# Kernel optimization log

Measured on AMD Instinct MI355X. Metric: run time of the kernel, lower is better.

Reference implementation:

```python
import jax, jax.numpy as jnp
import numpy as np
from jax import lax

WS = 8       # RSA window size
HEADS = 8    # GSA heads
EPS_LN = 1e-5

def conv1x1(x, w):  # x:(b,c,h,w), w:(o,c)
    return jnp.einsum('bchw,oc->bohw', x, w)

def dwconv3x3(x, w):  # w:(c,1,3,3) depthwise
    return lax.conv_general_dilated(x, w, (1, 1), ((1, 1), (1, 1)),
                                    dimension_numbers=('NCHW', 'OIHW', 'NCHW'),
                                    feature_group_count=x.shape[1])

def layernorm(x, w, b):  # WithBias LayerNorm over channel dim
    mu = x.mean(axis=1, keepdims=True)
    var = ((x - mu) ** 2).mean(axis=1, keepdims=True)
    return (x - mu) / jnp.sqrt(var + EPS_LN) * w[None, :, None, None] + b[None, :, None, None]

def l2norm(x):  # F.normalize(dim=-1)
    n = jnp.sqrt(jnp.sum(x * x, axis=-1, keepdims=True))
    return x / jnp.maximum(n, 1e-12)

def window_part(x, ws):  # (b,c,H,W) -> (b,nwin,ws*ws,c)
    b, c, H, W = x.shape
    x = x.reshape(b, c, H // ws, ws, W // ws, ws)
    x = x.transpose(0, 2, 4, 3, 5, 1)
    return x.reshape(b, (H // ws) * (W // ws), ws * ws, c)

def window_merge(x, ws, H, W):  # inverse of window_part
    b, nwin, _, c = x.shape
    x = x.reshape(b, H // ws, W // ws, ws, ws, c)
    x = x.transpose(0, 5, 1, 3, 2, 4)
    return x.reshape(b, c, H, W)

def rsa(x, qkv_w, dw_w, proj_w, temp):
    b, c, H, W = x.shape
    sh = WS // 2  # torch: roll by -wsize//2 = -4
    x_ = jnp.roll(x, (-sh, -sh), axis=(2, 3))
    qkv = dwconv3x3(conv1x1(x_, qkv_w), dw_w)
    q, k, v = jnp.split(qkv, 3, axis=1)
    q = l2norm(window_part(q, WS))
    k = l2norm(window_part(k, WS))
    v = window_part(v, WS)
    # attn[c,d] = sum_p q[p,c] k[p,d]; relu instead of softmax
    attn = jax.nn.relu(jnp.einsum('bnpc,bnpd->bncd', q, k) * temp[0, 0, 0])
    out = jnp.einsum('bnpc,bncd->bnpd', v, attn)
    out = window_merge(out, WS, H, W)
    out = jnp.roll(out, (sh, sh), axis=(2, 3))
    return conv1x1(out, proj_w), attn

def gsa(x, qkv_w, dw_w, proj_w, temp):
    b, c, H, W = x.shape
    cp = c // HEADS
    qkv = dwconv3x3(conv1x1(x, qkv_w), dw_w)
    q, k, v = jnp.split(qkv, 3, axis=1)
    heads = lambda t: t.reshape(b, HEADS, cp, H * W)
    q = l2norm(heads(q)); k = l2norm(heads(k)); v = heads(v)
    attn = jax.nn.relu(jnp.einsum('bhcn,bhdn->bhcd', q, k) * temp[0, 0, 0])
    out = jnp.einsum('bhcd,bhdn->bhcn', attn, v)  # (b,head,cp,HW)
    # rearrange 'b head c hw -> b (head c) h w' then 'b (head c) h w -> b (c head) h w'
    y = out.reshape(b, HEADS, cp, H, W).transpose(0, 2, 1, 3, 4).reshape(b, c, H, W)
    return conv1x1(y, proj_w), attn

def ffn(x, in_w, dw_w, out_w):  # Restormer gated-dconv FFN, bias=False
    h2 = dwconv3x3(conv1x1(x, in_w), dw_w)
    x1, x2 = jnp.split(h2, 2, axis=1)
    return conv1x1(jax.nn.gelu(x1, approximate=False) * x2, out_w)


def setup_inputs() -> dict:
    key = jax.random.key(0)
    B, C, H, W = 8, 64, 128, 128
    HID = int(C * 2.66)  # 170
    ks = jax.random.split(key, 20)
    g = lambda k, shp, s: (jax.random.normal(k, shp, dtype=jnp.float32) * s)
    d = {
        'x': g(ks[0], (B, C, H, W), 1.0),
        'ln_s0_w': jnp.ones((C,), jnp.float32), 'ln_s0_b': jnp.zeros((C,), jnp.float32),
        'ln_s2_w': jnp.ones((C,), jnp.float32), 'ln_s2_b': jnp.zeros((C,), jnp.float32),
        'rsa_qkv_w': g(ks[1], (3 * C, C), 0.05), 'rsa_dw_w': g(ks[2], (3 * C, 1, 3, 3), 0.1),
        'rsa_proj_w': g(ks[3], (C, C), 0.05), 'rsa_temp': jnp.ones((1, 1, 1), jnp.float32),
        'ffd_s_in_w': g(ks[4], (2 * HID, C), 0.05), 'ffd_s_dw_w': g(ks[5], (2 * HID, 1, 3, 3), 0.1),
        'ffd_s_out_w': g(ks[6], (C, HID), 0.05),
        'ln_c0_w': jnp.ones((C,), jnp.float32), 'ln_c0_b': jnp.zeros((C,), jnp.float32),
        'ln_c2_w': jnp.ones((C,), jnp.float32), 'ln_c2_b': jnp.zeros((C,), jnp.float32),
        'gsa_qkv_w': g(ks[7], (3 * C, C), 0.05), 'gsa_dw_w': g(ks[8], (3 * C, 1, 3, 3), 0.1),
        'gsa_proj_w': g(ks[9], (C, C), 0.05), 'gsa_temp': jnp.ones((1, 1, 1), jnp.float32),
        'ffd_c_in_w': g(ks[10], (2 * HID, C), 0.05), 'ffd_c_dw_w': g(ks[11], (2 * HID, 1, 3, 3), 0.1),
        'ffd_c_out_w': g(ks[12], (C, HID), 0.05),
    }
    return d


def reference(x, ln_s0_w, ln_s0_b, ln_s2_w, ln_s2_b,
              rsa_qkv_w, rsa_dw_w, rsa_proj_w, rsa_temp,
              ffd_s_in_w, ffd_s_dw_w, ffd_s_out_w,
              ln_c0_w, ln_c0_b, ln_c2_w, ln_c2_b,
              gsa_qkv_w, gsa_dw_w, gsa_proj_w, gsa_temp,
              ffd_c_in_w, ffd_c_dw_w, ffd_c_out_w):
    # FDT block, shared_depth=1 (i==0 branches only)
    x_, _ = rsa(layernorm(x, ln_s0_w, ln_s0_b), rsa_qkv_w, rsa_dw_w, rsa_proj_w, rsa_temp)
    x = ffn(layernorm(x_ + x, ln_s2_w, ln_s2_b), ffd_s_in_w, ffd_s_dw_w, ffd_s_out_w) + x_
    x_, _ = gsa(layernorm(x, ln_c0_w, ln_c0_b), gsa_qkv_w, gsa_dw_w, gsa_proj_w, gsa_temp)
    x = ffn(layernorm(x_ + x, ln_c2_w, ln_c2_b), ffd_c_in_w, ffd_c_dw_w, ffd_c_out_w) + x_
    return x
```

## Files before the change

kernel.cpp:

```cpp
#include <hip/hip_runtime.h>
#include <hip/hip_bf16.h>
#include <math.h>

#define DI __device__ __forceinline__

constexpr int B = 8, C = 64, H = 128, W = 128, N = H * W;
constexpr int HID = 170;
constexpr int QKVC = 3 * C;

typedef _Float16 half8 __attribute__((ext_vector_type(8)));
typedef _Float16 half4v __attribute__((ext_vector_type(4)));
typedef float f32x4 __attribute__((ext_vector_type(4)));

DI float gelu_fast(float v) {
    return v / (1.0f + __expf(-1.5957691216057308f * (v + 0.044715f * v * v * v)));
}

__global__ __launch_bounds__(64) void wpack_kernel(
    const float* __restrict__ Wm, const float* __restrict__ lnsc,
    int OREAL, int KREAL, int KT, _Float16* __restrict__ out)
{
    int f = blockIdx.x, l = threadIdx.x;
    int mt = f / KT, kt = f % KT;
    int row = mt * 16 + (l & 15);
    int col0 = kt * 32 + (l >> 4) * 8;
    half8 v;
#pragma unroll
    for (int i = 0; i < 8; ++i) {
        int col = col0 + i;
        float w = (row < OREAL && col < KREAL) ? Wm[row * KREAL + col] : 0.f;
        if (lnsc && col < KREAL) w *= lnsc[col];
        v[i] = (_Float16)w;
    }
    *(half8*)(out + (size_t)f * 512 + l * 8) = v;
}

__global__ __launch_bounds__(64) void wbias_kernel(
    const float* __restrict__ Wm, const float* __restrict__ lnb,
    int OREAL, int OPAD, float* __restrict__ biasv)
{
    int o = blockIdx.x * 64 + threadIdx.x;
    if (o >= OPAD) return;
    float s = 0.f;
    if (o < OREAL) {
#pragma unroll
        for (int c = 0; c < 64; ++c) s += Wm[o * 64 + c] * lnb[c];
    }
    biasv[o] = s;
}

__global__ __launch_bounds__(512) void weffpack_kernel(
    const float* __restrict__ weff, _Float16* __restrict__ out)
{
    int b = blockIdx.x;
    int f = threadIdx.x >> 6, l = threadIdx.x & 63;
    int mt = f >> 1, kt = f & 1;
    int row = mt * 16 + (l & 15);
    int col0 = kt * 32 + (l >> 4) * 8;
    const float* wb = weff + (size_t)b * 4096;
    half8 v;
#pragma unroll
    for (int i = 0; i < 8; ++i) v[i] = (_Float16)wb[row * 64 + col0 + i];
    *(half8*)(out + ((size_t)b * 8 + f) * 512 + l * 8) = v;
}

template<int MT, int OREAL, bool PRIM16, bool ADDIN>
__global__ __launch_bounds__(256, 1) void lngemm_kernel(
    const void* __restrict__ Xv, const float* __restrict__ Xadd,
    const float* __restrict__ biasv,
    const _Float16* __restrict__ Wp, _Float16* __restrict__ outp)
{
    __shared__ _Float16 stash[4][MT][16][66];
    int t = threadIdx.x, lane = t & 63, mg = t >> 6;
    int pbase = blockIdx.x * 64;
    int b = pbase >> 14, nb = pbase & (N - 1);
    int g = lane >> 4, lm = lane & 15;
    int krow0 = g * 8;

    half8 a[MT][2];
    const _Float16* wb = Wp + (size_t)(mg * MT * 2) * 512 + lane * 8;
#pragma unroll
    for (int mt = 0; mt < MT; ++mt)
#pragma unroll
        for (int kt = 0; kt < 2; ++kt)
            a[mt][kt] = *(const half8*)(wb + (mt * 2 + kt) * 512);

    int rowbase = mg * (MT * 16);
    const float* bp = biasv + rowbase + g * 4;

    const float*    xb32 = PRIM16 ? nullptr : ((const float*)Xv) + (size_t)b * 64 * N;
    const _Float16* xb16 = PRIM16 ? ((const _Float16*)Xv) + (size_t)b * 64 * N : nullptr;
    const float* ab = ADDIN ? (Xadd + (size_t)b * 64 * N) : nullptr;

#pragma unroll
    for (int cg = 0; cg < 4; ++cg) {
        int col = nb + cg * 16 + lm;
        float vv[2][8];
        float sm = 0.f, ss = 0.f;
#pragma unroll
        for (int kt = 0; kt < 2; ++kt)
#pragma unroll
            for (int i = 0; i < 8; ++i) {
                int c = kt * 32 + krow0 + i;
                float v = PRIM16 ? (float)xb16[(size_t)c * N + col] : xb32[(size_t)c * N + col];
                if (ADDIN) v += ab[(size_t)c * N + col];
                vv[kt][i] = v; sm += v; ss += v * v;
            }
        sm += __shfl_xor(sm, 16); ss += __shfl_xor(ss, 16);
        sm += __shfl_xor(sm, 32); ss += __shfl_xor(ss, 32);
        float mu = sm * (1.0f / 64.0f);
        float var = ss * (1.0f / 64.0f) - mu * mu;
        float rstd = rsqrtf(var + 1e-5f);
        half8 bf[2];
#pragma unroll
        for (int kt = 0; kt < 2; ++kt)
#pragma unroll
            for (int i = 0; i < 8; ++i)
                bf[kt][i] = (_Float16)((vv[kt][i] - mu) * rstd);

        f32x4 acc[MT];
#pragma unroll
        for (int mt = 0; mt < MT; ++mt) acc[mt] = *(const f32x4*)(bp + mt * 16);
#pragma unroll
        for (int kt = 0; kt < 2; ++kt)
#pragma unroll
            for (int mt = 0; mt < MT; ++mt)
                acc[mt] = __builtin_amdgcn_mfma_f32_16x16x32_f16(a[mt][kt], bf[kt], acc[mt], 0, 0, 0);

#pragma unroll
        for (int mt = 0; mt < MT; ++mt)
#pragma unroll
            for (int r = 0; r < 4; ++r)
                stash[mg][mt][g * 4 + r][cg * 16 + lm] = (_Float16)acc[mt][r];
    }
    __syncthreads();

    int row = lane >> 2, chunk = lane & 3;
#pragma unroll
    for (int mt = 0; mt < MT; ++mt) {
        int orow = rowbase + mt * 16 + row;
        if ((4 * MT * 16 == OREAL) || orow < OREAL) {
            half8 v0 = *(const half8*)&stash[mg][mt][row][chunk * 16];
            half8 v1 = *(const half8*)&stash[mg][mt][row][chunk * 16 + 8];
            _Float16* op = outp + ((size_t)b * OREAL + orow) * N + nb + chunk * 16;
            *(half8*)op = v0;
            *(half8*)(op + 8) = v1;
        }
    }
}

template<int MT, int KT, int MG, int NSTRIP, int CIN, int OREAL, int XROWS,
         bool PBW, bool OUT32, bool RESID>
__global__ __launch_bounds__(256, 1) void gemm_kernel(
    const _Float16* __restrict__ X, const _Float16* __restrict__ Wp,
    const _Float16* __restrict__ resid, void* __restrict__ outv)
{
    constexpr int PG = 4 / MG;
    constexpr int PPB = PG * 16 * NSTRIP;
    int t = threadIdx.x;
    int lane = t & 63, wv = t >> 6;
    int mg = wv % MG, pg = wv / MG;
    int pbase = blockIdx.x * PPB;
    int b = pbase >> 14, nb = pbase & (N - 1);

    half8 a[MT][KT];
    const _Float16* wb = Wp + ((size_t)(PBW ? b * (MG * MT * KT) : 0) + mg * MT * KT) * 512 + lane * 8;
#pragma unroll
    for (int mt = 0; mt < MT; ++mt)
#pragma unroll
        for (int kt = 0; kt < KT; ++kt)
            a[mt][kt] = *(const half8*)(wb + (mt * KT + kt) * 512);

    const _Float16* xb = X + (size_t)b * XROWS * N;
    int krow0 = (lane >> 4) * 8;

    for (int s = 0; s < NSTRIP; ++s) {
        int col = nb + (s * PG + pg) * 16 + (lane & 15);
        const _Float16* xp = xb + col;
        half8 bf[KT];
#pragma unroll
        for (int kt = 0; kt < KT; ++kt)
#pragma unroll
            for (int i = 0; i < 8; ++i) {
                int c = kt * 32 + krow0 + i;
                if (KT * 32 <= CIN || c < CIN) bf[kt][i] = xp[(size_t)c * N];
                else bf[kt][i] = (_Float16)0.f;
            }
        f32x4 acc[MT];
#pragma unroll
        for (int mt = 0; mt < MT; ++mt) acc[mt] = (f32x4){0.f, 0.f, 0.f, 0.f};
#pragma unroll
        for (int kt = 0; kt < KT; ++kt)
#pragma unroll
            for (int mt = 0; mt < MT; ++mt)
                acc[mt] = __builtin_amdgcn_mfma_f32_16x16x32_f16(a[mt][kt], bf[kt], acc[mt], 0, 0, 0);

        int orow0 = mg * (MT * 16) + (lane >> 4) * 4;
#pragma unroll
        for (int mt = 0; mt < MT; ++mt)
#pragma unroll
            for (int r = 0; r < 4; ++r) {
                int orow = orow0 + mt * 16 + r;
                bool ok = (MG * MT * 16 == OREAL) || (orow < OREAL);
                if (ok) {
                    size_t oidx = ((size_t)b * OREAL + orow) * N + col;
                    if constexpr (OUT32) {
                        float vv = acc[mt][r];
                        if constexpr (RESID) vv += (float)resid[((size_t)b * 64 + orow) * N + col];
                        ((float*)outv)[oidx] = vv;
                    } else {
                        ((_Float16*)outv)[oidx] = (_Float16)acc[mt][r];
                    }
                }
            }
    }
}

template<bool ROLLWM>
__global__ __launch_bounds__(256, 1) void dw16_kernel(
    const _Float16* __restrict__ in, const float* __restrict__ w,
    _Float16* __restrict__ out)
{
    int bc = blockIdx.y;
    int c = bc % 192;
    int n0 = (blockIdx.x * 256 + threadIdx.x) * 8;
    int y = n0 >> 7, x0 = n0 & 127;
    const _Float16* ib = in + (size_t)bc * N;
    const float* wr = w + c * 9;
    _Float16 wh[9];
#pragma unroll
    for (int i = 0; i < 9; ++i) wh[i] = (_Float16)wr[i];

    half8 acc = {0, 0, 0, 0, 0, 0, 0, 0};
#pragma unroll
    for (int r = 0; r < 3; ++r) {
        int yy = y - 1 + r;
        if (yy < 0 || yy > 127) continue;
        half8 sL, m, sR;
        if (!ROLLWM) {
            const _Float16* rp = ib + yy * W + x0;
            m = *(const half8*)rp;
            half8 pv = {0, 0, 0, 0, 0, 0, 0, 0};
            half8 nv = {0, 0, 0, 0, 0, 0, 0, 0};
            pv[7] = (x0 > 0) ? rp[-1] : (_Float16)0.f;
            nv[0] = (x0 < 120) ? rp[8] : (_Float16)0.f;
            sL = __builtin_shufflevector(pv, m, 7, 8, 9, 10, 11, 12, 13, 14);
            sR = __builtin_shufflevector(m, nv, 1, 2, 3, 4, 5, 6, 7, 8);
        } else {
            int sy = (yy + 4) & 127;
            const _Float16* rp = ib + sy * W;
            if (x0 <= 112) {
                half8 b0 = *(const half8*)(rp + x0);
                half8 b1 = *(const half8*)(rp + x0 + 8);
                sL = __builtin_shufflevector(b0, b1, 3, 4, 5, 6, 7, 8, 9, 10);
                m  = __builtin_shufflevector(b0, b1, 4, 5, 6, 7, 8, 9, 10, 11);
                sR = __builtin_shufflevector(b0, b1, 5, 6, 7, 8, 9, 10, 11, 12);
                if (x0 == 0) sL[0] = (_Float16)0.f;
            } else {
                _Float16 tmp[10];
#pragma unroll
                for (int j = 0; j < 10; ++j) {
                    int xx = 119 + j;
                    tmp[j] = (xx <= 127) ? rp[(xx + 4) & 127] : (_Float16)0.f;
                }
#pragma unroll
                for (int j = 0; j < 8; ++j) { sL[j] = tmp[j]; m[j] = tmp[j + 1]; sR[j] = tmp[j + 2]; }
            }
        }
        acc += sL * wh[r * 3 + 0] + m * wh[r * 3 + 1] + sR * wh[r * 3 + 2];
    }
    if (ROLLWM) {
        int win = ((y >> 3) << 4) | (x0 >> 3);
        int p = (y & 7) << 3;
        *(half8*)(out + (size_t)bc * N + win * 64 + p) = acc;
    } else {
        *(half8*)(out + (size_t)bc * N + n0) = acc;
    }
}

__global__ __launch_bounds__(256, 3) void rsa_win_kernel(
    const _Float16* __restrict__ qkv, const float* __restrict__ temp_p,
    const _Float16* __restrict__ pwp, _Float16* __restrict__ out)
{
    __shared__ _Float16 qT[64][72];
    __shared__ _Float16 kT[64][72];
    __shared__ _Float16 vP[64][76];
    __shared__ _Float16 aT[64][76];
    __shared__ _Float16 oP[64][76];
    __shared__ float tnorm[128];
    __shared__ _Float16 wsc[64];
    int blk = blockIdx.x, b = blk >> 8, win = blk & 255;
    int t = threadIdx.x, lane = t & 63, wv = t >> 6;
    int g = lane >> 4, lm = lane & 15;

    half8 pa0 = *(const half8*)(pwp + (size_t)(wv * 2 + 0) * 512 + lane * 8);
    half8 pa1 = *(const half8*)(pwp + (size_t)(wv * 2 + 1) * 512 + lane * 8);

    const _Float16* base = qkv + (size_t)b * QKVC * N + win * 64;
    {
        int c = t >> 2, q0 = (t & 3) * 16;
        const _Float16* pq = base + (size_t)c * N + q0;
        half8 a0 = *(const half8*)(pq);
        half8 a1 = *(const half8*)(pq + 8);
        *(half8*)&qT[c][q0] = a0;
        *(half8*)&qT[c][q0 + 8] = a1;
        const _Float16* pk = base + (size_t)(64 + c) * N + q0;
        half8 b0 = *(const half8*)(pk);
        half8 b1 = *(const half8*)(pk + 8);
        *(half8*)&kT[c][q0] = b0;
        *(half8*)&kT[c][q0 + 8] = b1;
        const _Float16* pv = base + (size_t)(128 + c) * N + q0;
        half8 v0 = *(const half8*)(pv);
        half8 v1 = *(const half8*)(pv + 8);
#pragma unroll
        for (int j = 0; j < 8; ++j) vP[q0 + j][c] = v0[j];
#pragma unroll
        for (int j = 0; j < 8; ++j) vP[q0 + 8 + j][c] = v1[j];
    }
    __syncthreads();
    if (t < 128) {
        int p = t & 63;
        float s = 0.f;
        if (t < 64) {
#pragma unroll
            for (int c = 0; c < 64; ++c) { float a = (float)qT[c][p]; s += a * a; }
        } else {
#pragma unroll
            for (int c = 0; c < 64; ++c) { float a = (float)kT[c][p]; s += a * a; }
        }
        tnorm[t] = s;
    }
    __syncthreads();
    if (t < 64) {
        float r = temp_p[0] / (fmaxf(sqrtf(tnorm[t]), 1e-12f) * fmaxf(sqrtf(tnorm[64 + t]), 1e-12f));
        wsc[t] = (_Float16)r;
    }
    __syncthreads();

    {
        half8 aq0 = *(const half8*)&qT[wv * 16 + lm][g * 8];
        half8 aq1 = *(const half8*)&qT[wv * 16 + lm][32 + g * 8];
        half8 ws0 = *(const half8*)&wsc[g * 8];
        half8 ws1 = *(const half8*)&wsc[32 + g * 8];
#pragma unroll
        for (int nt = 0; nt < 4; ++nt) {
            int d = nt * 16 + lm;
            half8 bk0 = *(const half8*)&kT[d][g * 8] * ws0;
            half8 bk1 = *(const half8*)&kT[d][32 + g * 8] * ws1;
            f32x4 acc = {0.f, 0.f, 0.f, 0.f};
            acc = __builtin_amdgcn_mfma_f32_16x16x32_f16(aq0, bk0, acc, 0, 0, 0);
            acc = __builtin_amdgcn_mfma_f32_16x16x32_f16(aq1, bk1, acc, 0, 0, 0);
#pragma unroll
            for (int r = 0; r < 4; ++r)
                aT[wv * 16 + g * 4 + r][d] = (_Float16)fmaxf(acc[r], 0.f);
        }
    }
    __syncthreads();

    {
        half8 a20, a21;
#pragma unroll
        for (int i = 0; i < 8; ++i) {
            a20[i] = aT[g * 8 + i][wv * 16 + lm];
            a21[i] = aT[32 + g * 8 + i][wv * 16 + lm];
        }
#pragma unroll
        for (int nt = 0; nt < 4; ++nt) {
            int p = nt * 16 + lm;
            half4v x0 = *(const half4v*)&vP[p][g * 8];
            half4v x1 = *(const half4v*)&vP[p][g * 8 + 4];
            half4v x2 = *(const half4v*)&vP[p][32 + g * 8];
            half4v x3 = *(const half4v*)&vP[p][32 + g * 8 + 4];
            half8 b20, b21;
#pragma unroll
            for (int j = 0; j < 4; ++j) { b20[j] = x0[j]; b20[4 + j] = x1[j]; b21[j] = x2[j]; b21[4 + j] = x3[j]; }
            f32x4 acc = {0.f, 0.f, 0.f, 0.f};
            acc = __builtin_amdgcn_mfma_f32_16x16x32_f16(a20, b20, acc, 0, 0, 0);
            acc = __builtin_amdgcn_mfma_f32_16x16x32_f16(a21, b21, acc, 0, 0, 0);
#pragma unroll
            for (int r = 0; r < 4; ++r)
                oP[p][wv * 16 + g * 4 + r] = (_Float16)acc[r];
        }
    }
    __syncthreads();

    {
        int y0 = (win >> 4) * 8, x0w = (win & 15) * 8;
        _Float16* ob = out + (size_t)b * C * N;
#pragma unroll
        for (int nt = 0; nt < 4; ++nt) {
            int p = nt * 16 + lm;
            half4v x0 = *(const half4v*)&oP[p][g * 8];
            half4v x1 = *(const half4v*)&oP[p][g * 8 + 4];
            half4v x2 = *(const half4v*)&oP[p][32 + g * 8];
            half4v x3 = *(const half4v*)&oP[p][32 + g * 8 + 4];
            half8 b30, b31;
#pragma unroll
            for (int j = 0; j < 4; ++j) { b30[j] = x0[j]; b30[4 + j] = x1[j]; b31[j] = x2[j]; b31[4 + j] = x3[j]; }
            f32x4 acc = {0.f, 0.f, 0.f, 0.f};
            acc = __builtin_amdgcn_mfma_f32_16x16x32_f16(pa0, b30, acc, 0, 0, 0);
            acc = __builtin_amdgcn_mfma_f32_16x16x32_f16(pa1, b31, acc, 0, 0, 0);
            int gy = (y0 + (p >> 3) + 4) & 127;
            int gx = (x0w + (p & 7) + 4) & 127;
#pragma unroll
            for (int r = 0; r < 4; ++r)
                ob[(size_t)(wv * 16 + g * 4 + r) * N + gy * W + gx] = (_Float16)acc[r];
        }
    }
}

__global__ __launch_bounds__(256, 1) void ffn_b_kernel(
    const _Float16* __restrict__ hid,
    const float* __restrict__ dww,
    _Float16* __restrict__ gated)
{
    int bc = blockIdx.y;
    int b = bc / 170, c = bc % 170;
    int n0 = (blockIdx.x * 256 + threadIdx.x) * 8;
    int y = n0 >> 7, x0 = n0 & 127;
    const _Float16* pa = hid + ((size_t)b * 340 + c) * N;
    const _Float16* pb = pa + (size_t)170 * N;
    const float* wa = dww + c * 9;
    const float* wbp = wa + 170 * 9;
    _Float16 wha[9], whb[9];
#pragma unroll
    for (int i = 0; i < 9; ++i) { wha[i] = (_Float16)wa[i]; whb[i] = (_Float16)wbp[i]; }

    half8 accA = {0, 0, 0, 0, 0, 0, 0, 0};
    half8 accB = {0, 0, 0, 0, 0, 0, 0, 0};
#pragma unroll
    for (int r = 0; r < 3; ++r) {
        int yy = y - 1 + r;
        if (yy < 0 || yy > 127) continue;
        {
            const _Float16* ra = pa + yy * W + x0;
            half8 m = *(const half8*)ra;
            half8 pv = {0, 0, 0, 0, 0, 0, 0, 0};
            half8 nv = {0, 0, 0, 0, 0, 0, 0, 0};
            pv[7] = (x0 > 0) ? ra[-1] : (_Float16)0.f;
            nv[0] = (x0 < 120) ? ra[8] : (_Float16)0.f;
            half8 sL = __builtin_shufflevector(pv, m, 7, 8, 9, 10, 11, 12, 13, 14);
            half8 sR = __builtin_shufflevector(m, nv, 1, 2, 3, 4, 5, 6, 7, 8);
            accA += sL * wha[r * 3 + 0] + m * wha[r * 3 + 1] + sR * wha[r * 3 + 2];
        }
        {
            const _Float16* rb = pb + yy * W + x0;
            half8 m = *(const half8*)rb;
            half8 pv = {0, 0, 0, 0, 0, 0, 0, 0};
            half8 nv = {0, 0, 0, 0, 0, 0, 0, 0};
            pv[7] = (x0 > 0) ? rb[-1] : (_Float16)0.f;
            nv[0] = (x0 < 120) ? rb[8] : (_Float16)0.f;
            half8 sL = __builtin_shufflevector(pv, m, 7, 8, 9, 10, 11, 12, 13, 14);
            half8 sR = __builtin_shufflevector(m, nv, 1, 2, 3, 4, 5, 6, 7, 8);
            accB += sL * whb[r * 3 + 0] + m * whb[r * 3 + 1] + sR * whb[r * 3 + 2];
        }
    }
    half8 o;
#pragma unroll
    for (int i = 0; i < 8; ++i) {
        float a = (float)accA[i];
        float g2 = (float)accB[i];
        o[i] = (_Float16)(gelu_fast(a) * g2);
    }
    *(half8*)(gated + ((size_t)b * 170 + c) * N + n0) = o;
}

__global__ __launch_bounds__(256, 1) void gsa_part_kernel(
    const _Float16* __restrict__ qkv, float* __restrict__ part)
{
    int bh = blockIdx.y, chunk = blockIdx.x;
    int b = bh >> 3, h = bh & 7;
    int t = threadIdx.x;
    const _Float16* qb = qkv + ((size_t)b * QKVC + h * 8) * N;
    const _Float16* kb = qb + (size_t)64 * N;
    float acc[80];
#pragma unroll
    for (int j = 0; j < 80; ++j) acc[j] = 0.f;
    for (int i = 0; i < 8; ++i) {
        int n = chunk * 2048 + i * 256 + t;
        float qv[8], kv[8];
#pragma unroll
        for (int c = 0; c < 8; ++c) { qv[c] = (float)qb[(size_t)c * N + n]; kv[c] = (float)kb[(size_t)c * N + n]; }
#pragma unroll
        for (int c = 0; c < 8; ++c) {
            acc[64 + c] += qv[c] * qv[c];
            acc[72 + c] += kv[c] * kv[c];
#pragma unroll
            for (int d = 0; d < 8; ++d) acc[c * 8 + d] += qv[c] * kv[d];
        }
    }
#pragma unroll
    for (int j = 0; j < 80; ++j) {
        float v = acc[j];
#pragma unroll
        for (int m = 1; m < 64; m <<= 1) v += __shfl_xor(v, m, 64);
        acc[j] = v;
    }
    __shared__ float red[4 * 80];
    if ((t & 63) == 0) {
#pragma unroll
        for (int j = 0; j < 80; ++j) red[(t >> 6) * 80 + j] = acc[j];
    }
    __syncthreads();
    if (t < 80) {
        float s = red[t] + red[80 + t] + red[160 + t] + red[240 + t];
        part[((size_t)bh * 8 + chunk) * 80 + t] = s;
    }
}

__global__ __launch_bounds__(128) void gsa_fin_kernel(
    const float* __restrict__ part, const float* __restrict__ temp_p,
    float* __restrict__ attn)
{
    int bh = blockIdx.x;
    int t = threadIdx.x;
    __shared__ float red[80];
    if (t < 80) {
        float s = 0.f;
        for (int ch = 0; ch < 8; ++ch) s += part[((size_t)bh * 8 + ch) * 80 + t];
        red[t] = s;
    }
    __syncthreads();
    if (t < 64) {
        int c = t >> 3, d = t & 7;
        float S  = red[c * 8 + d];
        float qn = fmaxf(sqrtf(red[64 + c]), 1e-12f);
        float kn = fmaxf(sqrtf(red[72 + d]), 1e-12f);
        attn[(size_t)bh * 64 + t] = fmaxf(temp_p[0] * S / (qn * kn), 0.f);
    }
}

__global__ __launch_bounds__(64) void weff_kernel(
    const float* __restrict__ attn, const float* __restrict__ pw,
    float* __restrict__ weff)
{
    int b = blockIdx.x;
    int o = threadIdx.x;
    __shared__ float al[512];
    for (int idx = o; idx < 512; idx += 64) al[idx] = attn[(size_t)b * 512 + idx];
    __syncthreads();
    for (int hd = 0; hd < 64; ++hd) {
        int h = hd >> 3, d = hd & 7;
        float acc = 0.f;
#pragma unroll
        for (int c = 0; c < 8; ++c)
            acc += pw[o * 64 + c * 8 + h] * al[h * 64 + c * 8 + d];
        weff[((size_t)b * 64 + o) * 64 + hd] = acc;
    }
}

__global__ void sentinel_kernel(float* out, int n) {
    int i = blockIdx.x * 256 + threadIdx.x;
    if (i < n) out[i] = 12345.0f;
}

extern "C" void kernel_launch(void* const* d_in, const int* in_sizes, int n_in,
                              void* d_out, int out_size, void* d_ws, size_t ws_size,
                              hipStream_t stream)
{
    const float* x         = (const float*)d_in[0];
    const float* ln_s0_w   = (const float*)d_in[1];
    const float* ln_s0_b   = (const float*)d_in[2];
    const float* ln_s2_w   = (const float*)d_in[3];
    const float* ln_s2_b   = (const float*)d_in[4];
    const float* rsa_qkv_w = (const float*)d_in[5];
    const float* rsa_dw_w  = (const float*)d_in[6];
    const float* rsa_proj_w= (const float*)d_in[7];
    const float* rsa_temp  = (const float*)d_in[8];
    const float* ffs_in_w  = (const float*)d_in[9];
    const float* ffs_dw_w  = (const float*)d_in[10];
    const float* ffs_out_w = (const float*)d_in[11];
    const float* ln_c0_w   = (const float*)d_in[12];
    const float* ln_c0_b   = (const float*)d_in[13];
    const float* ln_c2_w   = (const float*)d_in[14];
    const float* ln_c2_b   = (const float*)d_in[15];
    const float* gsa_qkv_w = (const float*)d_in[16];
    const float* gsa_dw_w  = (const float*)d_in[17];
    const float* gsa_proj_w= (const float*)d_in[18];
    const float* gsa_temp  = (const float*)d_in[19];
    const float* ffc_in_w  = (const float*)d_in[20];
    const float* ffc_dw_w  = (const float*)d_in[21];
    const float* ffc_out_w = (const float*)d_in[22];
    float* outp = (float*)d_out;

    char* ws = (char*)d_ws;
    _Float16* tmp192 = (_Float16*)(ws + 0);
    _Float16* Qbuf16 = (_Float16*)(ws + 50331648ull);
    _Float16* hidA   = (_Float16*)(ws + 0);
    _Float16* gated  = (_Float16*)(ws + 89128960ull);
    _Float16* wp_rsap= (_Float16*)(ws + 133693440ull);
    _Float16* S2h    = (_Float16*)(ws + 134217728ull);
    float*    part   = (float*)(ws + 167772160ull);
    float*    attn_s = (float*)(ws + 168427520ull);
    float*    weffb  = (float*)(ws + 168443904ull);
    _Float16* wp_rsa = (_Float16*)(ws + 168574976ull);
    _Float16* wp_gsa = (_Float16*)(ws + 168599552ull);
    _Float16* wp_fsi = (_Float16*)(ws + 168624128ull);
    _Float16* wp_fci = (_Float16*)(ws + 168673280ull);
    _Float16* wp_fso = (_Float16*)(ws + 168722432ull);
    _Float16* wp_fco = (_Float16*)(ws + 168747008ull);
    _Float16* wp_pbw = (_Float16*)(ws + 168771584ull);
    float*    wb_rsa = (float*)(ws + 168837120ull);
    float*    wb_gsa = (float*)(ws + 168838144ull);
    float*    wb_fsi = (float*)(ws + 168839168ull);
    float*    wb_fci = (float*)(ws + 168841216ull);
    if (ws_size < 168843264ull) {
        int n = out_size < 4096 ? out_size : 4096;
        sentinel_kernel<<<16, 256, 0, stream>>>(outp, n);
        return;
    }

    dim3 blk256(256);

    wpack_kernel<<<24, 64, 0, stream>>>(rsa_qkv_w, ln_s0_w, 192, 64, 2, wp_rsa);
    wpack_kernel<<<24, 64, 0, stream>>>(gsa_qkv_w, ln_c0_w, 192, 64, 2, wp_gsa);
    wpack_kernel<<<48, 64, 0, stream>>>(ffs_in_w, ln_s2_w, 340, 64, 2, wp_fsi);
    wpack_kernel<<<48, 64, 0, stream>>>(ffc_in_w, ln_c2_w, 340, 64, 2, wp_fci);
    wpack_kernel<<<24, 64, 0, stream>>>(ffs_out_w, nullptr, 64, 170, 6, wp_fso);
    wpack_kernel<<<24, 64, 0, stream>>>(ffc_out_w, nullptr, 64, 170, 6, wp_fco);
    wpack_kernel<<<8, 64, 0, stream>>>(rsa_proj_w, nullptr, 64, 64, 2, wp_rsap);
    wbias_kernel<<<3, 64, 0, stream>>>(rsa_qkv_w, ln_s0_b, 192, 192, wb_rsa);
    wbias_kernel<<<3, 64, 0, stream>>>(gsa_qkv_w, ln_c0_b, 192, 192, wb_gsa);
    wbias_kernel<<<6, 64, 0, stream>>>(ffs_in_w, ln_s2_b, 340, 384, wb_fsi);
    wbias_kernel<<<6, 64, 0, stream>>>(ffc_in_w, ln_c2_b, 340, 384, wb_fci);

    lngemm_kernel<3, 192, false, false><<<2048, blk256, 0, stream>>>(x, nullptr, wb_rsa, wp_rsa, tmp192);
    dw16_kernel<true><<<dim3(8, B * 192), blk256, 0, stream>>>(tmp192, rsa_dw_w, Qbuf16);
    rsa_win_kernel<<<2048, blk256, 0, stream>>>(Qbuf16, rsa_temp, wp_rsap, S2h);
    lngemm_kernel<6, 340, true, true><<<2048, blk256, 0, stream>>>(S2h, x, wb_fsi, wp_fsi, hidA);
    ffn_b_kernel<<<dim3(8, B * 170), blk256, 0, stream>>>(hidA, ffs_dw_w, gated);
    gemm_kernel<2, 6, 2, 2, 170, 64, 170, false, true, true>
        <<<2048, blk256, 0, stream>>>(gated, wp_fso, S2h, outp);

    lngemm_kernel<3, 192, false, false><<<2048, blk256, 0, stream>>>(outp, nullptr, wb_gsa, wp_gsa, tmp192);
    dw16_kernel<false><<<dim3(8, B * 192), blk256, 0, stream>>>(tmp192, gsa_dw_w, Qbuf16);
    gsa_part_kernel<<<dim3(8, 64), blk256, 0, stream>>>(Qbuf16, part);
    gsa_fin_kernel<<<64, dim3(128), 0, stream>>>(part, gsa_temp, attn_s);
    weff_kernel<<<8, dim3(64), 0, stream>>>(attn_s, gsa_proj_w, weffb);
    weffpack_kernel<<<8, dim3(512), 0, stream>>>(weffb, wp_pbw);
    gemm_kernel<4, 2, 1, 1, 64, 64, 192, true, false, false>
        <<<2048, blk256, 0, stream>>>(Qbuf16 + (size_t)128 * N, wp_pbw, nullptr, S2h);
    lngemm_kernel<6, 340, true, true><<<2048, blk256, 0, stream>>>(S2h, outp, wb_fci, wp_fci, hidA);
    ffn_b_kernel<<<dim3(8, B * 170), blk256, 0, stream>>>(hidA, ffc_dw_w, gated);
    gemm_kernel<2, 6, 2, 2, 170, 64, 170, false, true, true>
        <<<2048, blk256, 0, stream>>>(gated, wp_fco, S2h, outp);
}
```

Before: 393.4 us.

## Store intermediate block output in fp16 and widen FFN depthwise per-thread work

The first FFN output GEMM now writes the intermediate activation as fp16 (X2h) instead of fp32 into the output buffer. The following GSA layernorm-GEMM and the second FFN layernorm-GEMM read it as fp16, which halves traffic for that tensor. The FFN depthwise+gate kernel now processes 16 pixels per thread on a 3D grid, reusing halo loads and halving the block count. The fp16 intermediate adds rounding error to the residual path.

```diff
diff --git a/kernel.cpp b/kernel.cpp
--- a/kernel.cpp
+++ b/kernel.cpp
@@ -64,9 +64,9 @@
     *(half8*)(out + ((size_t)b * 8 + f) * 512 + l * 8) = v;
 }
 
-template<int MT, int OREAL, bool PRIM16, bool ADDIN>
+template<int MT, int OREAL, bool PRIM16, bool RES16, bool ADDIN>
 __global__ __launch_bounds__(256, 1) void lngemm_kernel(
-    const void* __restrict__ Xv, const float* __restrict__ Xadd,
+    const void* __restrict__ Xv, const void* __restrict__ Xaddv,
     const float* __restrict__ biasv,
     const _Float16* __restrict__ Wp, _Float16* __restrict__ outp)
 {
@@ -90,7 +90,8 @@
 
     const float*    xb32 = PRIM16 ? nullptr : ((const float*)Xv) + (size_t)b * 64 * N;
     const _Float16* xb16 = PRIM16 ? ((const _Float16*)Xv) + (size_t)b * 64 * N : nullptr;
-    const float* ab = ADDIN ? (Xadd + (size_t)b * 64 * N) : nullptr;
+    const float*    ab32 = (ADDIN && !RES16) ? ((const float*)Xaddv) + (size_t)b * 64 * N : nullptr;
+    const _Float16* ab16 = (ADDIN && RES16) ? ((const _Float16*)Xaddv) + (size_t)b * 64 * N : nullptr;
 
 #pragma unroll
     for (int cg = 0; cg < 4; ++cg) {
@@ -103,7 +104,7 @@
             for (int i = 0; i < 8; ++i) {
                 int c = kt * 32 + krow0 + i;
                 float v = PRIM16 ? (float)xb16[(size_t)c * N + col] : xb32[(size_t)c * N + col];
-                if (ADDIN) v += ab[(size_t)c * N + col];
+                if (ADDIN) v += RES16 ? (float)ab16[(size_t)c * N + col] : ab32[(size_t)c * N + col];
                 vv[kt][i] = v; sm += v; ss += v * v;
             }
         sm += __shfl_xor(sm, 16); ss += __shfl_xor(ss, 16);
@@ -204,13 +205,10 @@
                 bool ok = (MG * MT * 16 == OREAL) || (orow < OREAL);
                 if (ok) {
                     size_t oidx = ((size_t)b * OREAL + orow) * N + col;
-                    if constexpr (OUT32) {
-                        float vv = acc[mt][r];
-                        if constexpr (RESID) vv += (float)resid[((size_t)b * 64 + orow) * N + col];
-                        ((float*)outv)[oidx] = vv;
-                    } else {
-                        ((_Float16*)outv)[oidx] = (_Float16)acc[mt][r];
-                    }
+                    float vv = acc[mt][r];
+                    if constexpr (RESID) vv += (float)resid[((size_t)b * 64 + orow) * N + col];
+                    if constexpr (OUT32) ((float*)outv)[oidx] = vv;
+                    else                 ((_Float16*)outv)[oidx] = (_Float16)vv;
                 }
             }
     }
@@ -414,9 +412,8 @@
     const float* __restrict__ dww,
     _Float16* __restrict__ gated)
 {
-    int bc = blockIdx.y;
-    int b = bc / 170, c = bc % 170;
-    int n0 = (blockIdx.x * 256 + threadIdx.x) * 8;
+    int c = blockIdx.y, b = blockIdx.z;
+    int n0 = (blockIdx.x * 256 + threadIdx.x) * 16;
     int y = n0 >> 7, x0 = n0 & 127;
     const _Float16* pa = hid + ((size_t)b * 340 + c) * N;
     const _Float16* pb = pa + (size_t)170 * N;
@@ -426,43 +423,52 @@
 #pragma unroll
     for (int i = 0; i < 9; ++i) { wha[i] = (_Float16)wa[i]; whb[i] = (_Float16)wbp[i]; }
 
-    half8 accA = {0, 0, 0, 0, 0, 0, 0, 0};
-    half8 accB = {0, 0, 0, 0, 0, 0, 0, 0};
+    half8 aA0 = {0,0,0,0,0,0,0,0}, aA1 = {0,0,0,0,0,0,0,0};
+    half8 aB0 = {0,0,0,0,0,0,0,0}, aB1 = {0,0,0,0,0,0,0,0};
 #pragma unroll
     for (int r = 0; r < 3; ++r) {
         int yy = y - 1 + r;
         if (yy < 0 || yy > 127) continue;
         {
             const _Float16* ra = pa + yy * W + x0;
-            half8 m = *(const half8*)ra;
-            half8 pv = {0, 0, 0, 0, 0, 0, 0, 0};
-            half8 nv = {0, 0, 0, 0, 0, 0, 0, 0};
-            pv[7] = (x0 > 0) ? ra[-1] : (_Float16)0.f;
-            nv[0] = (x0 < 120) ? ra[8] : (_Float16)0.f;
-            half8 sL = __builtin_shufflevector(pv, m, 7, 8, 9, 10, 11, 12, 13, 14);
-            half8 sR = __builtin_shufflevector(m, nv, 1, 2, 3, 4, 5, 6, 7, 8);
-            accA += sL * wha[r * 3 + 0] + m * wha[r * 3 + 1] + sR * wha[r * 3 + 2];
+            half8 m0 = *(const half8*)ra;
+            half8 m1 = *(const half8*)(ra + 8);
+            half8 pv = {0,0,0,0,0,0,0,0};
+            half8 nv = {0,0,0,0,0,0,0,0};
+            pv[7] = (x0 > 0)   ? ra[-1] : (_Float16)0.f;
+            nv[0] = (x0 < 112) ? ra[16] : (_Float16)0.f;
+            half8 sL0 = __builtin_shufflevector(pv, m0, 7, 8, 9, 10, 11, 12, 13, 14);
+            half8 sR0 = __builtin_shufflevector(m0, m1, 1, 2, 3, 4, 5, 6, 7, 8);
+            half8 sL1 = __builtin_shufflevector(m0, m1, 7, 8, 9, 10, 11, 12, 13, 14);
+            half8 sR1 = __builtin_shufflevector(m1, nv, 1, 2, 3, 4, 5, 6, 7, 8);
+            aA0 += sL0 * wha[r * 3 + 0] + m0 * wha[r * 3 + 1] + sR0 * wha[r * 3 + 2];
+            aA1 += sL1 * wha[r * 3 + 0] + m1 * wha[r * 3 + 1] + sR1 * wha[r * 3 + 2];
         }
         {
             const _Float16* rb = pb + yy * W + x0;
-            half8 m = *(const half8*)rb;
-            half8 pv = {0, 0, 0, 0, 0, 0, 0, 0};
-            half8 nv = {0, 0, 0, 0, 0, 0, 0, 0};
-            pv[7] = (x0 > 0) ? rb[-1] : (_Float16)0.f;
-            nv[0] = (x0 < 120) ? rb[8] : (_Float16)0.f;
-            half8 sL = __builtin_shufflevector(pv, m, 7, 8, 9, 10, 11, 12, 13, 14);
-            half8 sR = __builtin_shufflevector(m, nv, 1, 2, 3, 4, 5, 6, 7, 8);
-            accB += sL * whb[r * 3 + 0] + m * whb[r * 3 + 1] + sR * whb[r * 3 + 2];
-        }
-    }
-    half8 o;
+            half8 m0 = *(const half8*)rb;
+            half8 m1 = *(const half8*)(rb + 8);
+            half8 pv = {0,0,0,0,0,0,0,0};
+            half8 nv = {0,0,0,0,0,0,0,0};
+            pv[7] = (x0 > 0)   ? rb[-1] : (_Float16)0.f;
+            nv[0] = (x0 < 112) ? rb[16] : (_Float16)0.f;
+            half8 sL0 = __builtin_shufflevector(pv, m0, 7, 8, 9, 10, 11, 12, 13, 14);
+            half8 sR0 = __builtin_shufflevector(m0, m1, 1, 2, 3, 4, 5, 6, 7, 8);
+            half8 sL1 = __builtin_shufflevector(m0, m1, 7, 8, 9, 10, 11, 12, 13, 14);
+            half8 sR1 = __builtin_shufflevector(m1, nv, 1, 2, 3, 4, 5, 6, 7, 8);
+            aB0 += sL0 * whb[r * 3 + 0] + m0 * whb[r * 3 + 1] + sR0 * whb[r * 3 + 2];
+            aB1 += sL1 * whb[r * 3 + 0] + m1 * whb[r * 3 + 1] + sR1 * whb[r * 3 + 2];
+        }
+    }
+    half8 o0, o1;
 #pragma unroll
     for (int i = 0; i < 8; ++i) {
-        float a = (float)accA[i];
-        float g2 = (float)accB[i];
-        o[i] = (_Float16)(gelu_fast(a) * g2);
-    }
-    *(half8*)(gated + ((size_t)b * 170 + c) * N + n0) = o;
+        o0[i] = (_Float16)(gelu_fast((float)aA0[i]) * (float)aB0[i]);
+        o1[i] = (_Float16)(gelu_fast((float)aA1[i]) * (float)aB1[i]);
+    }
+    _Float16* op = gated + ((size_t)b * 170 + c) * N + n0;
+    *(half8*)op = o0;
+    *(half8*)(op + 8) = o1;
 }
 
 __global__ __launch_bounds__(256, 1) void gsa_part_kernel(
@@ -590,6 +596,7 @@
     _Float16* gated  = (_Float16*)(ws + 89128960ull);
     _Float16* wp_rsap= (_Float16*)(ws + 133693440ull);
     _Float16* S2h    = (_Float16*)(ws + 134217728ull);
+    _Float16* X2h    = (_Float16*)(ws + 150994944ull);
     float*    part   = (float*)(ws + 167772160ull);
     float*    attn_s = (float*)(ws + 168427520ull);
     float*    weffb  = (float*)(ws + 168443904ull);
@@ -624,15 +631,15 @@
     wbias_kernel<<<6, 64, 0, stream>>>(ffs_in_w, ln_s2_b, 340, 384, wb_fsi);
     wbias_kernel<<<6, 64, 0, stream>>>(ffc_in_w, ln_c2_b, 340, 384, wb_fci);
 
-    lngemm_kernel<3, 192, false, false><<<2048, blk256, 0, stream>>>(x, nullptr, wb_rsa, wp_rsa, tmp192);
+    lngemm_kernel<3, 192, false, false, false><<<2048, blk256, 0, stream>>>(x, nullptr, wb_rsa, wp_rsa, tmp192);
     dw16_kernel<true><<<dim3(8, B * 192), blk256, 0, stream>>>(tmp192, rsa_dw_w, Qbuf16);
     rsa_win_kernel<<<2048, blk256, 0, stream>>>(Qbuf16, rsa_temp, wp_rsap, S2h);
-    lngemm_kernel<6, 340, true, true><<<2048, blk256, 0, stream>>>(S2h, x, wb_fsi, wp_fsi, hidA);
-    ffn_b_kernel<<<dim3(8, B * 170), blk256, 0, stream>>>(hidA, ffs_dw_w, gated);
-    gemm_kernel<2, 6, 2, 2, 170, 64, 170, false, true, true>
-        <<<2048, blk256, 0, stream>>>(gated, wp_fso, S2h, outp);
-
-    lngemm_kernel<3, 192, false, false><<<2048, blk256, 0, stream>>>(outp, nullptr, wb_gsa, wp_gsa, tmp192);
+    lngemm_kernel<6, 340, true, false, true><<<2048, blk256, 0, stream>>>(S2h, x, wb_fsi, wp_fsi, hidA);
+    ffn_b_kernel<<<dim3(4, 170, B), blk256, 0, stream>>>(hidA, ffs_dw_w, gated);
+    gemm_kernel<2, 6, 2, 2, 170, 64, 170, false, false, true>
+        <<<2048, blk256, 0, stream>>>(gated, wp_fso, S2h, X2h);
+
+    lngemm_kernel<3, 192, true, false, false><<<2048, blk256, 0, stream>>>(X2h, nullptr, wb_gsa, wp_gsa, tmp192);
     dw16_kernel<false><<<dim3(8, B * 192), blk256, 0, stream>>>(tmp192, gsa_dw_w, Qbuf16);
     gsa_part_kernel<<<dim3(8, 64), blk256, 0, stream>>>(Qbuf16, part);
     gsa_fin_kernel<<<64, dim3(128), 0, stream>>>(part, gsa_temp, attn_s);
@@ -640,8 +647,8 @@
     weffpack_kernel<<<8, dim3(512), 0, stream>>>(weffb, wp_pbw);
     gemm_kernel<4, 2, 1, 1, 64, 64, 192, true, false, false>
         <<<2048, blk256, 0, stream>>>(Qbuf16 + (size_t)128 * N, wp_pbw, nullptr, S2h);
-    lngemm_kernel<6, 340, true, true><<<2048, blk256, 0, stream>>>(S2h, outp, wb_fci, wp_fci, hidA);
-    ffn_b_kernel<<<dim3(8, B * 170), blk256, 0, stream>>>(hidA, ffc_dw_w, gated);
+    lngemm_kernel<6, 340, true, true, true><<<2048, blk256, 0, stream>>>(S2h, X2h, wb_fci, wp_fci, hidA);
+    ffn_b_kernel<<<dim3(4, 170, B), blk256, 0, stream>>>(hidA, ffc_dw_w, gated);
     gemm_kernel<2, 6, 2, 2, 170, 64, 170, false, true, true>
         <<<2048, blk256, 0, stream>>>(gated, wp_fco, S2h, outp);
 }
```

After: 404.4 us. 2.8% more time.

## Store 64-channel activations pixel-major in fp16 for vectorized LN-GEMM loads

Applied to the files above, without the earlier changes.

Adds a transpose kernel that converts the fp32 NCHW input into fp16 pixel-major (NHWC) layout. The LN-GEMM kernels, the RSA window kernel output, the GEMM residual reads and the intermediate block output now all use this layout, so each lane reads or writes contiguous half8/half4 vectors. The intermediate residual stream is also kept in fp16 instead of fp32. This is meant to cut memory traffic and scattered per-channel accesses. The cost is an extra transpose pass and reduced precision of the residual stream between the two halves of the block.

```diff
diff --git a/kernel.cpp b/kernel.cpp
--- a/kernel.cpp
+++ b/kernel.cpp
@@ -64,9 +64,39 @@
     *(half8*)(out + ((size_t)b * 8 + f) * 512 + l * 8) = v;
 }
 
-template<int MT, int OREAL, bool PRIM16, bool ADDIN>
+__global__ __launch_bounds__(256, 1) void xpose_kernel(
+    const float* __restrict__ x, _Float16* __restrict__ xT)
+{
+    __shared__ _Float16 tile[64][72];
+    int blk = blockIdx.x;
+    int b = blk >> 8, tb = blk & 255;
+    int n0 = tb * 64;
+    int t = threadIdx.x;
+    {
+        int ch = t >> 2, seg = t & 3;
+        const float* xp = x + ((size_t)b * 64 + ch) * N + n0 + seg * 16;
+#pragma unroll
+        for (int jj = 0; jj < 4; ++jj) {
+            f32x4 v = *(const f32x4*)(xp + jj * 4);
+#pragma unroll
+            for (int k = 0; k < 4; ++k)
+                tile[seg * 16 + jj * 4 + k][ch] = (_Float16)v[k];
+        }
+    }
+    __syncthreads();
+    {
+        int px = t >> 2, part = t & 3;
+        half8 h0 = *(const half8*)&tile[px][part * 16];
+        half8 h1 = *(const half8*)&tile[px][part * 16 + 8];
+        _Float16* op = xT + ((size_t)b * N + n0 + px) * 64 + part * 16;
+        *(half8*)op = h0;
+        *(half8*)(op + 8) = h1;
+    }
+}
+
+template<int MT, int OREAL, bool ADDIN>
 __global__ __launch_bounds__(256, 1) void lngemm_kernel(
-    const void* __restrict__ Xv, const float* __restrict__ Xadd,
+    const _Float16* __restrict__ Xp, const _Float16* __restrict__ Rp,
     const float* __restrict__ biasv,
     const _Float16* __restrict__ Wp, _Float16* __restrict__ outp)
 {
@@ -88,24 +118,36 @@
     int rowbase = mg * (MT * 16);
     const float* bp = biasv + rowbase + g * 4;
 
-    const float*    xb32 = PRIM16 ? nullptr : ((const float*)Xv) + (size_t)b * 64 * N;
-    const _Float16* xb16 = PRIM16 ? ((const _Float16*)Xv) + (size_t)b * 64 * N : nullptr;
-    const float* ab = ADDIN ? (Xadd + (size_t)b * 64 * N) : nullptr;
+    const _Float16* xb = Xp + (size_t)b * N * 64;
+    const _Float16* ab = ADDIN ? (Rp + (size_t)b * N * 64) : nullptr;
 
 #pragma unroll
     for (int cg = 0; cg < 4; ++cg) {
         int col = nb + cg * 16 + lm;
+        const _Float16* xp = xb + (size_t)col * 64;
+        half8 h0 = *(const half8*)(xp + krow0);
+        half8 h1 = *(const half8*)(xp + 32 + krow0);
         float vv[2][8];
         float sm = 0.f, ss = 0.f;
-#pragma unroll
-        for (int kt = 0; kt < 2; ++kt)
+        if (ADDIN) {
+            const _Float16* ap = ab + (size_t)col * 64;
+            half8 r0 = *(const half8*)(ap + krow0);
+            half8 r1 = *(const half8*)(ap + 32 + krow0);
 #pragma unroll
             for (int i = 0; i < 8; ++i) {
-                int c = kt * 32 + krow0 + i;
-                float v = PRIM16 ? (float)xb16[(size_t)c * N + col] : xb32[(size_t)c * N + col];
-                if (ADDIN) v += ab[(size_t)c * N + col];
-                vv[kt][i] = v; sm += v; ss += v * v;
+                float v0 = (float)h0[i] + (float)r0[i];
+                float v1 = (float)h1[i] + (float)r1[i];
+                vv[0][i] = v0; vv[1][i] = v1;
+                sm += v0 + v1; ss += v0 * v0 + v1 * v1;
             }
+        } else {
+#pragma unroll
+            for (int i = 0; i < 8; ++i) {
+                float v0 = (float)h0[i], v1 = (float)h1[i];
+                vv[0][i] = v0; vv[1][i] = v1;
+                sm += v0 + v1; ss += v0 * v0 + v1 * v1;
+            }
+        }
         sm += __shfl_xor(sm, 16); ss += __shfl_xor(ss, 16);
         sm += __shfl_xor(sm, 32); ss += __shfl_xor(ss, 32);
         float mu = sm * (1.0f / 64.0f);
@@ -197,22 +239,29 @@
 
         int orow0 = mg * (MT * 16) + (lane >> 4) * 4;
 #pragma unroll
-        for (int mt = 0; mt < MT; ++mt)
-#pragma unroll
-            for (int r = 0; r < 4; ++r) {
-                int orow = orow0 + mt * 16 + r;
-                bool ok = (MG * MT * 16 == OREAL) || (orow < OREAL);
-                if (ok) {
-                    size_t oidx = ((size_t)b * OREAL + orow) * N + col;
-                    if constexpr (OUT32) {
-                        float vv = acc[mt][r];
-                        if constexpr (RESID) vv += (float)resid[((size_t)b * 64 + orow) * N + col];
-                        ((float*)outv)[oidx] = vv;
-                    } else {
-                        ((_Float16*)outv)[oidx] = (_Float16)acc[mt][r];
-                    }
+        for (int mt = 0; mt < MT; ++mt) {
+            int ob0 = orow0 + mt * 16;
+            half4v res;
+            if constexpr (RESID)
+                res = *(const half4v*)(resid + ((size_t)b * N + col) * 64 + ob0);
+            if constexpr (OUT32) {
+#pragma unroll
+                for (int r = 0; r < 4; ++r) {
+                    float vv = acc[mt][r];
+                    if constexpr (RESID) vv += (float)res[r];
+                    ((float*)outv)[((size_t)b * OREAL + ob0 + r) * N + col] = vv;
                 }
+            } else {
+                half4v h;
+#pragma unroll
+                for (int r = 0; r < 4; ++r) {
+                    float vv = acc[mt][r];
+                    if constexpr (RESID) vv += (float)res[r];
+                    h[r] = (_Float16)vv;
+                }
+                *(half4v*)((_Float16*)outv + ((size_t)b * N + col) * 64 + ob0) = h;
             }
+        }
     }
 }
 
@@ -386,7 +435,7 @@
 
     {
         int y0 = (win >> 4) * 8, x0w = (win & 15) * 8;
-        _Float16* ob = out + (size_t)b * C * N;
+        _Float16* ob = out + (size_t)b * N * 64;
 #pragma unroll
         for (int nt = 0; nt < 4; ++nt) {
             int p = nt * 16 + lm;
@@ -402,9 +451,10 @@
             acc = __builtin_amdgcn_mfma_f32_16x16x32_f16(pa1, b31, acc, 0, 0, 0);
             int gy = (y0 + (p >> 3) + 4) & 127;
             int gx = (x0w + (p & 7) + 4) & 127;
-#pragma unroll
-            for (int r = 0; r < 4; ++r)
-                ob[(size_t)(wv * 16 + g * 4 + r) * N + gy * W + gx] = (_Float16)acc[r];
+            half4v h;
+#pragma unroll
+            for (int r = 0; r < 4; ++r) h[r] = (_Float16)acc[r];
+            *(half4v*)(ob + (size_t)(gy * W + gx) * 64 + wv * 16 + g * 4) = h;
         }
     }
 }
@@ -414,8 +464,7 @@
     const float* __restrict__ dww,
     _Float16* __restrict__ gated)
 {
-    int bc = blockIdx.y;
-    int b = bc / 170, c = bc % 170;
+    int c = blockIdx.y, b = blockIdx.z;
     int n0 = (blockIdx.x * 256 + threadIdx.x) * 8;
     int y = n0 >> 7, x0 = n0 & 127;
     const _Float16* pa = hid + ((size_t)b * 340 + c) * N;
@@ -457,11 +506,8 @@
     }
     half8 o;
 #pragma unroll
-    for (int i = 0; i < 8; ++i) {
-        float a = (float)accA[i];
-        float g2 = (float)accB[i];
-        o[i] = (_Float16)(gelu_fast(a) * g2);
-    }
+    for (int i = 0; i < 8; ++i)
+        o[i] = (_Float16)(gelu_fast((float)accA[i]) * (float)accB[i]);
     *(half8*)(gated + ((size_t)b * 170 + c) * N + n0) = o;
 }
 
@@ -590,6 +636,8 @@
     _Float16* gated  = (_Float16*)(ws + 89128960ull);
     _Float16* wp_rsap= (_Float16*)(ws + 133693440ull);
     _Float16* S2h    = (_Float16*)(ws + 134217728ull);
+    _Float16* X2h    = (_Float16*)(ws + 150994944ull);
+    _Float16* xT     = X2h;
     float*    part   = (float*)(ws + 167772160ull);
     float*    attn_s = (float*)(ws + 168427520ull);
     float*    weffb  = (float*)(ws + 168443904ull);
@@ -624,15 +672,16 @@
     wbias_kernel<<<6, 64, 0, stream>>>(ffs_in_w, ln_s2_b, 340, 384, wb_fsi);
     wbias_kernel<<<6, 64, 0, stream>>>(ffc_in_w, ln_c2_b, 340, 384, wb_fci);
 
-    lngemm_kernel<3, 192, false, false><<<2048, blk256, 0, stream>>>(x, nullptr, wb_rsa, wp_rsa, tmp192);
+    xpose_kernel<<<2048, blk256, 0, stream>>>(x, xT);
+    lngemm_kernel<3, 192, false><<<2048, blk256, 0, stream>>>(xT, nullptr, wb_rsa, wp_rsa, tmp192);
     dw16_kernel<true><<<dim3(8, B * 192), blk256, 0, stream>>>(tmp192, rsa_dw_w, Qbuf16);
     rsa_win_kernel<<<2048, blk256, 0, stream>>>(Qbuf16, rsa_temp, wp_rsap, S2h);
-    lngemm_kernel<6, 340, true, true><<<2048, blk256, 0, stream>>>(S2h, x, wb_fsi, wp_fsi, hidA);
-    ffn_b_kernel<<<dim3(8, B * 170), blk256, 0, stream>>>(hidA, ffs_dw_w, gated);
-    gemm_kernel<2, 6, 2, 2, 170, 64, 170, false, true, true>
-        <<<2048, blk256, 0, stream>>>(gated, wp_fso, S2h, outp);
-
-    lngemm_kernel<3, 192, false, false><<<2048, blk256, 0, stream>>>(outp, nullptr, wb_gsa, wp_gsa, tmp192);
+    lngemm_kernel<6, 340, true><<<2048, blk256, 0, stream>>>(S2h, xT, wb_fsi, wp_fsi, hidA);
+    ffn_b_kernel<<<dim3(8, 170, B), blk256, 0, stream>>>(hidA, ffs_dw_w, gated);
+    gemm_kernel<2, 6, 2, 2, 170, 64, 170, false, false, true>
+        <<<2048, blk256, 0, stream>>>(gated, wp_fso, S2h, X2h);
+
+    lngemm_kernel<3, 192, false><<<2048, blk256, 0, stream>>>(X2h, nullptr, wb_gsa, wp_gsa, tmp192);
     dw16_kernel<false><<<dim3(8, B * 192), blk256, 0, stream>>>(tmp192, gsa_dw_w, Qbuf16);
     gsa_part_kernel<<<dim3(8, 64), blk256, 0, stream>>>(Qbuf16, part);
     gsa_fin_kernel<<<64, dim3(128), 0, stream>>>(part, gsa_temp, attn_s);
@@ -640,8 +689,8 @@
     weffpack_kernel<<<8, dim3(512), 0, stream>>>(weffb, wp_pbw);
     gemm_kernel<4, 2, 1, 1, 64, 64, 192, true, false, false>
         <<<2048, blk256, 0, stream>>>(Qbuf16 + (size_t)128 * N, wp_pbw, nullptr, S2h);
-    lngemm_kernel<6, 340, true, true><<<2048, blk256, 0, stream>>>(S2h, outp, wb_fci, wp_fci, hidA);
-    ffn_b_kernel<<<dim3(8, B * 170), blk256, 0, stream>>>(hidA, ffc_dw_w, gated);
+    lngemm_kernel<6, 340, true><<<2048, blk256, 0, stream>>>(S2h, X2h, wb_fci, wp_fci, hidA);
+    ffn_b_kernel<<<dim3(8, 170, B), blk256, 0, stream>>>(hidA, ffc_dw_w, gated);
     gemm_kernel<2, 6, 2, 2, 170, 64, 170, false, true, true>
         <<<2048, blk256, 0, stream>>>(gated, wp_fco, S2h, outp);
 }
```

New measurement: 391.6 us. No clear change (-0.4%).
